# Kernel optimization log

Measured on AMD Instinct MI355X. Metric: run time of the kernel, lower is better.

## Reference

```python
import jax, jax.numpy as jnp
import numpy as np

N_SUM, N_MAX, M, HID, OUT, E, L = 2048, 64, 16, 128, 64, 16384, 4


def setup_inputs() -> dict:
    key = jax.random.key(0)
    ks = jax.random.split(key, 8)
    inp = {}
    inp["W"] = jax.random.normal(ks[0], (N_SUM, N_MAX, M), jnp.float32)
    inp["mask"] = jnp.ones((N_SUM, N_MAX), jnp.float32)
    inp["src"] = jax.random.randint(ks[1], (E,), 0, N_SUM)
    inp["dst"] = jax.random.randint(ks[2], (E,), 0, N_SUM)
    # GIN parameters: per-layer eps, MLP (Linear -> BN -> ReLU -> Linear)
    inp["eps"] = jax.random.normal(ks[3], (L,), jnp.float32)
    inp["W1_first"] = jax.random.normal(ks[4], (M, HID), jnp.float32) / np.sqrt(M).astype(np.float32)
    inp["b1_first"] = jnp.zeros((HID,), jnp.float32)
    inp["W1_rest"] = jax.random.normal(ks[5], (L - 1, HID, HID), jnp.float32) / np.sqrt(HID).astype(np.float32)
    inp["b1_rest"] = jnp.zeros((L - 1, HID), jnp.float32)
    inp["bn_gamma"] = jnp.ones((L, HID), jnp.float32)
    inp["bn_beta"] = jnp.zeros((L, HID), jnp.float32)
    inp["W2_mid"] = jax.random.normal(ks[6], (L - 1, HID, HID), jnp.float32) / np.sqrt(HID).astype(np.float32)
    inp["b2_mid"] = jnp.zeros((L - 1, HID), jnp.float32)
    inp["W2_last"] = jax.random.normal(ks[7], (HID, OUT), jnp.float32) / np.sqrt(HID).astype(np.float32)
    inp["b2_last"] = jnp.zeros((OUT,), jnp.float32)
    return inp


def _batchnorm(Hf, gamma, beta):
    # training-mode BatchNorm1d over flattened leading dims (biased variance)
    mu = Hf.mean(axis=0)
    var = Hf.var(axis=0)
    return (Hf - mu) * jax.lax.rsqrt(var + 1e-5) * gamma + beta


def _gin_layer(X, src, dst, eps, W1, b1, gamma, beta, W2, b2):
    # scatter-add message passing: gather sources, segment-sum into targets
    S = jax.ops.segment_sum(X[src], dst, num_segments=X.shape[0])  # [N_sum, n_max, D]
    Z = (1.0 + eps) * X + S
    H = Z @ W1 + b1                     # [N_sum, n_max, HID]
    shp = H.shape
    H = _batchnorm(H.reshape(-1, shp[-1]), gamma, beta)
    H = jax.nn.relu(H).reshape(shp)
    return H @ W2 + b2


def reference(W, mask, src, dst, eps, W1_first, b1_first, W1_rest, b1_rest,
              bn_gamma, bn_beta, W2_mid, b2_mid, W2_last, b2_last):
    X = W
    for l in range(L):
        W1 = W1_first if l == 0 else W1_rest[l - 1]
        b1 = b1_first if l == 0 else b1_rest[l - 1]
        W2 = W2_mid[l] if l < L - 1 else W2_last
        b2 = b2_mid[l] if l < L - 1 else b2_last
        X = _gin_layer(X, src, dst, eps[l], W1, b1, bn_gamma[l], bn_beta[l], W2, b2)
    # masked sum over the padded node axis -> positional encodings [N_sum, OUT]
    PE = (X * mask[:, :, None]).sum(axis=1)
    return PE
```

## Files before the change

kernel.cpp:

```cpp
#include <hip/hip_runtime.h>

#define N_SUM 2048
#define HIDD 128
#define NEDGE 16384
#define ROWS (N_SUM * 64)
#define NSLOT 16

typedef short short8 __attribute__((ext_vector_type(8)));
typedef float floatx4 __attribute__((ext_vector_type(4)));
typedef unsigned int uint4n __attribute__((ext_vector_type(4)));
typedef unsigned short ushort_t;

__device__ __forceinline__ ushort_t f2bf(float f) {
    unsigned u = __builtin_bit_cast(unsigned, f);
    u += 0x7fffu + ((u >> 16) & 1u);
    return (ushort_t)(u >> 16);
}
__device__ __forceinline__ float bf2f(ushort_t h) {
    return __builtin_bit_cast(float, (unsigned)h << 16);
}
__device__ __forceinline__ void unpack8(uint4 v, float* f) {
    f[0] = bf2f(v.x & 0xffff); f[1] = bf2f(v.x >> 16);
    f[2] = bf2f(v.y & 0xffff); f[3] = bf2f(v.y >> 16);
    f[4] = bf2f(v.z & 0xffff); f[5] = bf2f(v.z >> 16);
    f[6] = bf2f(v.w & 0xffff); f[7] = bf2f(v.w >> 16);
}
__device__ __forceinline__ uint4 pack8(const float* f) {
    uint4 v;
    v.x = f2bf(f[0]) | ((unsigned)f2bf(f[1]) << 16);
    v.y = f2bf(f[2]) | ((unsigned)f2bf(f[3]) << 16);
    v.z = f2bf(f[4]) | ((unsigned)f2bf(f[5]) << 16);
    v.w = f2bf(f[6]) | ((unsigned)f2bf(f[7]) << 16);
    return v;
}
__device__ __forceinline__ void nt_store16(const void* src, void* dst) {
    __builtin_nontemporal_store(*(const uint4n*)src, (uint4n*)dst);
}

__global__ __launch_bounds__(1024) void mega_prep(const int* __restrict__ src, const int* __restrict__ dst,
                                                  const float* __restrict__ W1f, const float* __restrict__ W2l,
                                                  const float* __restrict__ b2m, const float* __restrict__ W1r,
                                                  const float* __restrict__ W2m,
                                                  int* __restrict__ irp, int* __restrict__ icol,
                                                  ushort_t* __restrict__ w1t0, ushort_t* __restrict__ w2lt,
                                                  float* __restrict__ bvec, ushort_t* __restrict__ w21t,
                                                  float* __restrict__ sums) {
    __shared__ int sdeg[2048];
    __shared__ int scur[2048];
    __shared__ int red[1024];
    int tid = threadIdx.x, blk = blockIdx.x;

    if (blk == 0) {
        sdeg[tid] = 0;
        sdeg[tid + 1024] = 0;
        __syncthreads();
        int d[16];
#pragma unroll
        for (int q = 0; q < 16; q++) d[q] = dst[q * 1024 + tid];
#pragma unroll
        for (int q = 0; q < 16; q++) atomicAdd(&sdeg[d[q]], 1);
        __syncthreads();
        int a = sdeg[2 * tid], b = sdeg[2 * tid + 1];
        red[tid] = a + b;
        __syncthreads();
        for (int off = 1; off < 1024; off <<= 1) {
            int v = (tid >= off) ? red[tid - off] : 0;
            __syncthreads();
            red[tid] += v;
            __syncthreads();
        }
        int base = (tid == 0) ? 0 : red[tid - 1];
        irp[2 * tid] = base;
        irp[2 * tid + 1] = base + a;
        scur[2 * tid] = base;
        scur[2 * tid + 1] = base + a;
        if (tid == 1023) irp[2048] = red[1023];
        __syncthreads();
        int s[16];
#pragma unroll
        for (int q = 0; q < 16; q++) s[q] = src[q * 1024 + tid];
#pragma unroll
        for (int q = 0; q < 16; q++) {
            int pos = atomicAdd(&scur[d[q]], 1);
            icol[pos] = s[q];
        }
    } else if (blk <= 13) {
        int idx = (blk - 1) * 1024 + tid;
        if (idx < 4096) {
            int nn = idx >> 5, k = idx & 31;
            w1t0[idx] = f2bf(k < 16 ? W1f[k * 128 + nn] : 0.f);
        } else if (idx < 4096 + 8192) {
            int r = idx - 4096;
            int nn = r >> 7, k = r & 127;
            w2lt[r] = f2bf(W2l[k * 64 + nn]);
        } else if (idx < 4096 + 8192 + 384) {
            int r = idx - 12288;
            int lm = r >> 7, c = r & 127;
            float s = 0.f;
            for (int o = 0; o < 128; o++) s += b2m[lm * 128 + o] * W1r[(size_t)lm * 16384 + o * 128 + c];
            bvec[r] = s;
        }
    } else if (blk <= 61) {
        int idx = (blk - 14) * 1024 + tid;
        int lm = idx >> 14, r = idx & 16383, i = r >> 7, c = r & 127;
        const float* w2row = W2m + (size_t)lm * 16384 + i * 128;
        const float* w1col = W1r + (size_t)lm * 16384 + c;
        float s = 0.f;
#pragma unroll 8
        for (int o = 0; o < 128; o++) s += w2row[o] * w1col[o * 128];
        w21t[(size_t)lm * 16384 + c * 128 + i] = f2bf(s);
    } else {
        int idx = (blk - 62) * 1024 + tid;
#pragma unroll
        for (int q = 0; q < 8; q++) sums[idx * 8 + q] = 0.f;
    }
}


__global__ __launch_bounds__(256, 4) void gin_mm1_l0(const float* __restrict__ Xf, const ushort_t* __restrict__ W1t,
                                                     const float* __restrict__ b1, const float* __restrict__ eps,
                                                     const int* __restrict__ rp, const int* __restrict__ colv,
                                                     ushort_t* __restrict__ H, float* __restrict__ sums) {
    __shared__ ushort_t Zs[64 * 128];
    int tid = threadIdx.x, n = blockIdx.x;
    float ev = 1.0f + eps[0];
    int e0 = rp[n], e1 = rp[n + 1], deg = e1 - e0;
    const float4* X = (const float4*)Xf;

    float4 sA, sB;
    sA = X[(size_t)n * 256 + tid];
    if (deg > 0) sB = X[(size_t)colv[e0] * 256 + tid];
    float4 a;
    a.x = sA.x * ev; a.y = sA.y * ev; a.z = sA.z * ev; a.w = sA.w * ev;
    int i = 1;
    for (; i + 1 < deg; i += 2) {
        sA = X[(size_t)colv[e0 + i] * 256 + tid];
        a.x += sB.x; a.y += sB.y; a.z += sB.z; a.w += sB.w;
        sB = X[(size_t)colv[e0 + i + 1] * 256 + tid];
        a.x += sA.x; a.y += sA.y; a.z += sA.z; a.w += sA.w;
    }
    if (deg > 0) {
        if (i < deg) {
            sA = X[(size_t)colv[e0 + i] * 256 + tid];
            a.x += sB.x; a.y += sB.y; a.z += sB.z; a.w += sB.w;
            a.x += sA.x; a.y += sA.y; a.z += sA.z; a.w += sA.w;
        } else {
            a.x += sB.x; a.y += sB.y; a.z += sB.z; a.w += sB.w;
        }
    }

    {
        int m = tid >> 2, k0 = (tid & 3) * 4;
        int addr = ((k0 >> 3) * 64 + m) * 8 + (k0 & 7);
        uint2 pv;
        pv.x = f2bf(a.x) | ((unsigned)f2bf(a.y) << 16);
        pv.y = f2bf(a.z) | ((unsigned)f2bf(a.w) << 16);
        *(uint2*)&Zs[addr] = pv;
        *(uint2*)&Zs[1024 + tid * 4] = make_uint2(0u, 0u);
    }
    __syncthreads();

    int w = tid >> 6, lane = tid & 63, lg = lane >> 4, ln = lane & 15;
    floatx4 C[4][2];
#pragma unroll
    for (int mt = 0; mt < 4; mt++) { C[mt][0] = {0.f, 0.f, 0.f, 0.f}; C[mt][1] = {0.f, 0.f, 0.f, 0.f}; }

    {
        short8 B0 = *(const short8*)&W1t[(w * 32 + ln) * 32 + lg * 8];
        short8 B1 = *(const short8*)&W1t[(w * 32 + 16 + ln) * 32 + lg * 8];
#pragma unroll
        for (int mt = 0; mt < 4; mt++) {
            short8 A = *(const short8*)&Zs[(lg * 64 + mt * 16 + ln) * 8];
            C[mt][0] = __builtin_amdgcn_mfma_f32_16x16x32_bf16(A, B0, C[mt][0], 0, 0, 0);
            C[mt][1] = __builtin_amdgcn_mfma_f32_16x16x32_bf16(A, B1, C[mt][1], 0, 0, 0);
        }
    }

    float bsum[2], bsq[2];
    float bv[2] = {b1[w * 32 + ln], b1[w * 32 + 16 + ln]};
#pragma unroll
    for (int nt = 0; nt < 2; nt++) {
        float s = 0.f, s2 = 0.f;
#pragma unroll
        for (int mt = 0; mt < 4; mt++)
#pragma unroll
            for (int r = 0; r < 4; r++) {
                float v = C[mt][nt][r] + bv[nt];
                C[mt][nt][r] = v;
                s += v; s2 += v * v;
            }
        bsum[nt] = s; bsq[nt] = s2;
    }
#pragma unroll
    for (int nt = 0; nt < 2; nt++) {
        bsum[nt] += __shfl_xor(bsum[nt], 16, 64);
        bsum[nt] += __shfl_xor(bsum[nt], 32, 64);
        bsq[nt] += __shfl_xor(bsq[nt], 16, 64);
        bsq[nt] += __shfl_xor(bsq[nt], 32, 64);
    }
    if (lg == 0) {
        float* sl = sums + (n & (NSLOT - 1)) * 256;
        int c0 = w * 32 + ln;
        atomicAdd(&sl[c0], bsum[0]);
        atomicAdd(&sl[c0 + 16], bsum[1]);
        atomicAdd(&sl[128 + c0], bsq[0]);
        atomicAdd(&sl[128 + c0 + 16], bsq[1]);
    }
    __syncthreads();
#pragma unroll
    for (int nt = 0; nt < 2; nt++) {
        int colc = w * 32 + nt * 16 + ln;
        int base = (colc >> 3) * 512 + (colc & 7);
#pragma unroll
        for (int mt = 0; mt < 4; mt++)
#pragma unroll
            for (int r = 0; r < 4; r++) {
                int row = mt * 16 + lg * 4 + r;
                Zs[base + row * 8] = f2bf(C[mt][nt][r]);
            }
    }
    __syncthreads();
#pragma unroll
    for (int q = 0; q < 4; q++)
        nt_store16(&((const uint4*)Zs)[q * 256 + tid], &((uint4*)&H[(size_t)n * 8192])[q * 256 + tid]);
}

__global__ __launch_bounds__(512, 4) void gin_mm1_fused(const ushort_t* __restrict__ Hin,
                                                        const ushort_t* __restrict__ W21t,
                                                        const float* __restrict__ b1, const float* __restrict__ bvec,
                                                        const float* __restrict__ sums_prev,
                                                        const float* __restrict__ gam_prev,
                                                        const float* __restrict__ bet_prev,
                                                        const float* __restrict__ epsp,
                                                        const int* __restrict__ rp, const int* __restrict__ colv,
                                                        ushort_t* __restrict__ Hout, float* __restrict__ sums_cur) {
    __shared__ ushort_t Zs[64 * 128];
    __shared__ float scs_lds[256];
    int tid = threadIdx.x, n = blockIdx.x;
    if (tid < 128) {
        float s = 0.f, s2 = 0.f;
#pragma unroll
        for (int k = 0; k < NSLOT; k++) {
            s += sums_prev[k * 256 + tid];
            s2 += sums_prev[k * 256 + 128 + tid];
        }
        float mean = s * (1.f / (float)ROWS);
        float var = s2 * (1.f / (float)ROWS) - mean * mean;
        float sc = gam_prev[tid] * rsqrtf(var + 1e-5f);
        scs_lds[tid] = sc;
        scs_lds[128 + tid] = bet_prev[tid] - mean * sc;
    }
    __syncthreads();

    unsigned scp[2][8];
#pragma unroll
    for (int q = 0; q < 2; q++) {
        int cb = ((q * 512 + tid) >> 6) * 8;
#pragma unroll
        for (int j = 0; j < 8; j++)
            scp[q][j] = ((unsigned)f2bf(scs_lds[cb + j])) | ((unsigned)f2bf(scs_lds[128 + cb + j]) << 16);
    }

    float ev = 1.0f + epsp[0];
    int e0 = rp[n], e1 = rp[n + 1], deg = e1 - e0;
    const uint4* X = (const uint4*)Hin;
    float acc[2][8];
    uint4 bufA[2], bufB[2];

    auto loadslab = [&](uint4* buf, int node) {
        const uint4* p = X + (size_t)node * 1024;
        buf[0] = p[tid];
        buf[1] = p[512 + tid];
    };
    auto addp = [&](const uint4* buf) {
#pragma unroll
        for (int q = 0; q < 2; q++) {
            float f[8]; unpack8(buf[q], f);
#pragma unroll
            for (int j = 0; j < 8; j++) {
                float sc = __builtin_bit_cast(float, scp[q][j] << 16);
                float sh = __builtin_bit_cast(float, scp[q][j] & 0xffff0000u);
                acc[q][j] += fmaxf(fmaf(f[j], sc, sh), 0.f);
            }
        }
    };

    loadslab(bufA, n);
    if (deg > 0) loadslab(bufB, colv[e0]);

#pragma unroll
    for (int q = 0; q < 2; q++) {
        float f[8]; unpack8(bufA[q], f);
#pragma unroll
        for (int j = 0; j < 8; j++) {
            float sc = __builtin_bit_cast(float, scp[q][j] << 16);
            float sh = __builtin_bit_cast(float, scp[q][j] & 0xffff0000u);
            acc[q][j] = ev * fmaxf(fmaf(f[j], sc, sh), 0.f);
        }
    }

    int i = 1;
    for (; i + 1 < deg; i += 2) {
        loadslab(bufA, colv[e0 + i]);
        addp(bufB);
        loadslab(bufB, colv[e0 + i + 1]);
        addp(bufA);
    }
    if (deg > 0) {
        if (i < deg) {
            loadslab(bufA, colv[e0 + i]);
            addp(bufB);
            addp(bufA);
        } else {
            addp(bufB);
        }
    }

#pragma unroll
    for (int q = 0; q < 2; q++) ((uint4*)Zs)[q * 512 + tid] = pack8(acc[q]);
    __syncthreads();

    int w = tid >> 6, lane = tid & 63, lg = lane >> 4, ln = lane & 15;
    floatx4 C[4];
#pragma unroll
    for (int mt = 0; mt < 4; mt++) C[mt] = {0.f, 0.f, 0.f, 0.f};

    for (int kb = 0; kb < 4; kb++) {
        short8 B = *(const short8*)&W21t[(w * 16 + ln) * 128 + kb * 32 + lg * 8];
#pragma unroll
        for (int mt = 0; mt < 4; mt++) {
            short8 A = *(const short8*)&Zs[((kb * 4 + lg) * 64 + mt * 16 + ln) * 8];
            C[mt] = __builtin_amdgcn_mfma_f32_16x16x32_bf16(A, B, C[mt], 0, 0, 0);
        }
    }

    float fac = ev + (float)deg;
    int c0 = w * 16 + ln;
    float bv = b1[c0] + fac * bvec[c0];
    float s = 0.f, s2 = 0.f;
#pragma unroll
    for (int mt = 0; mt < 4; mt++)
#pragma unroll
        for (int r = 0; r < 4; r++) {
            float v = C[mt][r] + bv;
            C[mt][r] = v;
            s += v; s2 += v * v;
        }
    s += __shfl_xor(s, 16, 64);
    s += __shfl_xor(s, 32, 64);
    s2 += __shfl_xor(s2, 16, 64);
    s2 += __shfl_xor(s2, 32, 64);
    if (lg == 0) {
        float* sl = sums_cur + (n & (NSLOT - 1)) * 256;
        atomicAdd(&sl[c0], s);
        atomicAdd(&sl[128 + c0], s2);
    }

    __syncthreads();
    {
        int base = (c0 >> 3) * 512 + (c0 & 7);
#pragma unroll
        for (int mt = 0; mt < 4; mt++)
#pragma unroll
            for (int r = 0; r < 4; r++) {
                int row = mt * 16 + lg * 4 + r;
                Zs[base + row * 8] = f2bf(C[mt][r]);
            }
    }
    __syncthreads();
#pragma unroll
    for (int q = 0; q < 2; q++)
        nt_store16(&((const uint4*)Zs)[q * 512 + tid], &((uint4*)&Hout[(size_t)n * 8192])[q * 512 + tid]);
}

__global__ __launch_bounds__(256, 4) void gin_mm2_last(const ushort_t* __restrict__ H, const ushort_t* __restrict__ W2t,
                                                       const float* __restrict__ b2,
                                                       const float* __restrict__ sums_prev,
                                                       const float* __restrict__ gam_prev,
                                                       const float* __restrict__ bet_prev,
                                                       const float* __restrict__ mask, float* __restrict__ out) {
    __shared__ ushort_t Hs[64 * 128];
    __shared__ float scs_lds[256];
    int tid = threadIdx.x, n = blockIdx.x;
    if (tid < 128) {
        float s = 0.f, s2 = 0.f;
#pragma unroll
        for (int k = 0; k < NSLOT; k++) {
            s += sums_prev[k * 256 + tid];
            s2 += sums_prev[k * 256 + 128 + tid];
        }
        float mean = s * (1.f / (float)ROWS);
        float var = s2 * (1.f / (float)ROWS) - mean * mean;
        float sc = gam_prev[tid] * rsqrtf(var + 1e-5f);
        scs_lds[tid] = sc;
        scs_lds[128 + tid] = bet_prev[tid] - mean * sc;
    }
    __syncthreads();

#pragma unroll
    for (int q = 0; q < 4; q++) {
        int c = q * 256 + tid;
        uint4 v = ((const uint4*)&H[(size_t)n * 8192])[c];
        float f[8]; unpack8(v, f);
        int cb = (c >> 6) * 8;
#pragma unroll
        for (int j = 0; j < 8; j++) f[j] = fmaxf(fmaf(f[j], scs_lds[cb + j], scs_lds[128 + cb + j]), 0.f);
        ((uint4*)Hs)[c] = pack8(f);
    }
    __syncthreads();

    int w = tid >> 6, lane = tid & 63, lg = lane >> 4, ln = lane & 15;
    floatx4 C[4];
#pragma unroll
    for (int mt = 0; mt < 4; mt++) C[mt] = {0.f, 0.f, 0.f, 0.f};

    for (int kb = 0; kb < 4; kb++) {
        short8 B = *(const short8*)&W2t[(w * 16 + ln) * 128 + kb * 32 + lg * 8];
#pragma unroll
        for (int mt = 0; mt < 4; mt++) {
            short8 A = *(const short8*)&Hs[((kb * 4 + lg) * 64 + mt * 16 + ln) * 8];
            C[mt] = __builtin_amdgcn_mfma_f32_16x16x32_bf16(A, B, C[mt], 0, 0, 0);
        }
    }

    int colc = w * 16 + ln;
    float bb = b2[colc];
    float pe = 0.f;
#pragma unroll
    for (int mt = 0; mt < 4; mt++)
#pragma unroll
        for (int r = 0; r < 4; r++) {
            int row = mt * 16 + lg * 4 + r;
            pe += mask[n * 64 + row] * (C[mt][r] + bb);
        }
    pe += __shfl_xor(pe, 16, 64);
    pe += __shfl_xor(pe, 32, 64);
    if (lg == 0) out[(size_t)n * 64 + colc] = pe;
}

extern "C" void kernel_launch(void* const* d_in, const int* in_sizes, int n_in, void* d_out, int out_size,
                              void* d_ws, size_t ws_size, hipStream_t stream) {
    const float* W    = (const float*)d_in[0];
    const float* mask = (const float*)d_in[1];
    const int* src    = (const int*)d_in[2];
    const int* dst    = (const int*)d_in[3];
    const float* eps  = (const float*)d_in[4];
    const float* W1f  = (const float*)d_in[5];
    const float* b1f  = (const float*)d_in[6];
    const float* W1r  = (const float*)d_in[7];
    const float* b1r  = (const float*)d_in[8];
    const float* gam  = (const float*)d_in[9];
    const float* bet  = (const float*)d_in[10];
    const float* W2m  = (const float*)d_in[11];
    const float* b2m  = (const float*)d_in[12];
    const float* W2l  = (const float*)d_in[13];
    const float* b2l  = (const float*)d_in[14];
    float* out = (float*)d_out;

    ushort_t* Ha   = (ushort_t*)d_ws;
    ushort_t* Hb   = Ha + 16777216;
    ushort_t* w1t0 = Hb + 16777216;
    ushort_t* w2lt = w1t0 + 4096;
    ushort_t* w21t = w2lt + 8192;
    float* bvec    = (float*)(w21t + 49152);
    float* sums    = bvec + 384;
    int* irp       = (int*)(sums + 16384);
    int* icol      = irp + 2052;

    mega_prep<<<64, 1024, 0, stream>>>(src, dst, W1f, W2l, b2m, W1r, W2m, irp, icol,
                                       w1t0, w2lt, bvec, w21t, sums);

    const int SL = NSLOT * 256;
    gin_mm1_l0<<<N_SUM, 256, 0, stream>>>(W, w1t0, b1f, eps, irp, icol, Ha, sums);
    gin_mm1_fused<<<N_SUM, 512, 0, stream>>>(Ha, w21t, b1r, bvec, sums, gam, bet, eps + 1,
                                             irp, icol, Hb, sums + SL);
    gin_mm1_fused<<<N_SUM, 512, 0, stream>>>(Hb, w21t + 16384, b1r + 128, bvec + 128, sums + SL,
                                             gam + 128, bet + 128, eps + 2, irp, icol, Ha, sums + 2 * SL);
    gin_mm1_fused<<<N_SUM, 512, 0, stream>>>(Ha, w21t + 32768, b1r + 256, bvec + 256, sums + 2 * SL,
                                             gam + 256, bet + 256, eps + 3, irp, icol, Hb, sums + 3 * SL);
    gin_mm2_last<<<N_SUM, 256, 0, stream>>>(Hb, w2lt, b2l, sums + 3 * SL, gam + 384, bet + 384, mask, out);
}
```

Before: 263.7 us.

## Pad CSR neighbor lists to multiples of four and gather four slabs in flight

Each node's adjacency list is padded to a multiple of four with a sentinel node index that points to an all-zero slab appended to each H buffer. The fused layer kernels now keep four neighbor slab loads in flight instead of two, so more memory latency is overlapped during the gather. Padded entries go through the BN/ReLU transform like real neighbors, and their contribution (relu of the shift term) is subtracted afterwards using the true degree. The cost is extra gather traffic for the padding, larger register use, and a small amount of extra setup work in the prep kernel.

```diff
diff --git a/kernel.cpp b/kernel.cpp
--- a/kernel.cpp
+++ b/kernel.cpp
@@ -5,6 +5,8 @@
 #define NEDGE 16384
 #define ROWS (N_SUM * 64)
 #define NSLOT 16
+#define SLAB 8192
+#define SENT 2048
 
 typedef short short8 __attribute__((ext_vector_type(8)));
 typedef float floatx4 __attribute__((ext_vector_type(4)));
@@ -42,9 +44,11 @@
                                                   const float* __restrict__ b2m, const float* __restrict__ W1r,
                                                   const float* __restrict__ W2m,
                                                   int* __restrict__ irp, int* __restrict__ icol,
+                                                  int* __restrict__ idegv,
                                                   ushort_t* __restrict__ w1t0, ushort_t* __restrict__ w2lt,
                                                   float* __restrict__ bvec, ushort_t* __restrict__ w21t,
-                                                  float* __restrict__ sums) {
+                                                  float* __restrict__ sums,
+                                                  ushort_t* __restrict__ Ha, ushort_t* __restrict__ Hb) {
     __shared__ int sdeg[2048];
     __shared__ int scur[2048];
     __shared__ int red[1024];
@@ -61,7 +65,8 @@
         for (int q = 0; q < 16; q++) atomicAdd(&sdeg[d[q]], 1);
         __syncthreads();
         int a = sdeg[2 * tid], b = sdeg[2 * tid + 1];
-        red[tid] = a + b;
+        int ap = (a + 3) & ~3, bp = (b + 3) & ~3;
+        red[tid] = ap + bp;
         __syncthreads();
         for (int off = 1; off < 1024; off <<= 1) {
             int v = (tid >= off) ? red[tid - off] : 0;
@@ -71,9 +76,13 @@
         }
         int base = (tid == 0) ? 0 : red[tid - 1];
         irp[2 * tid] = base;
-        irp[2 * tid + 1] = base + a;
+        irp[2 * tid + 1] = base + ap;
         scur[2 * tid] = base;
-        scur[2 * tid + 1] = base + a;
+        scur[2 * tid + 1] = base + ap;
+        idegv[2 * tid] = a;
+        idegv[2 * tid + 1] = b;
+        sdeg[2 * tid] = base + ap;
+        sdeg[2 * tid + 1] = base + ap + bp;
         if (tid == 1023) irp[2048] = red[1023];
         __syncthreads();
         int s[16];
@@ -83,6 +92,12 @@
         for (int q = 0; q < 16; q++) {
             int pos = atomicAdd(&scur[d[q]], 1);
             icol[pos] = s[q];
+        }
+        __syncthreads();
+#pragma unroll
+        for (int q = 0; q < 2; q++) {
+            int node = 2 * tid + q;
+            for (int p = scur[node]; p < sdeg[node]; p++) icol[p] = SENT;
         }
     } else if (blk <= 13) {
         int idx = (blk - 1) * 1024 + tid;
@@ -109,22 +124,26 @@
 #pragma unroll 8
         for (int o = 0; o < 128; o++) s += w2row[o] * w1col[o * 128];
         w21t[(size_t)lm * 16384 + c * 128 + i] = f2bf(s);
+    } else if (blk == 62) {
+#pragma unroll
+        for (int q = 0; q < 16; q++) sums[tid * 16 + q] = 0.f;
     } else {
-        int idx = (blk - 62) * 1024 + tid;
-#pragma unroll
-        for (int q = 0; q < 8; q++) sums[idx * 8 + q] = 0.f;
+        uint4 z = make_uint4(0u, 0u, 0u, 0u);
+        ((uint4*)(Ha + (size_t)SENT * SLAB))[tid] = z;
+        ((uint4*)(Hb + (size_t)SENT * SLAB))[tid] = z;
     }
 }
 
 
 __global__ __launch_bounds__(256, 4) void gin_mm1_l0(const float* __restrict__ Xf, const ushort_t* __restrict__ W1t,
                                                      const float* __restrict__ b1, const float* __restrict__ eps,
-                                                     const int* __restrict__ rp, const int* __restrict__ colv,
+                                                     const int* __restrict__ rp, const int* __restrict__ idegv,
+                                                     const int* __restrict__ colv,
                                                      ushort_t* __restrict__ H, float* __restrict__ sums) {
     __shared__ ushort_t Zs[64 * 128];
     int tid = threadIdx.x, n = blockIdx.x;
     float ev = 1.0f + eps[0];
-    int e0 = rp[n], e1 = rp[n + 1], deg = e1 - e0;
+    int e0 = rp[n], deg = idegv[n];
     const float4* X = (const float4*)Xf;
 
     float4 sA, sB;
@@ -222,7 +241,7 @@
     __syncthreads();
 #pragma unroll
     for (int q = 0; q < 4; q++)
-        nt_store16(&((const uint4*)Zs)[q * 256 + tid], &((uint4*)&H[(size_t)n * 8192])[q * 256 + tid]);
+        nt_store16(&((const uint4*)Zs)[q * 256 + tid], &((uint4*)&H[(size_t)n * SLAB])[q * 256 + tid]);
 }
 
 __global__ __launch_bounds__(512, 4) void gin_mm1_fused(const ushort_t* __restrict__ Hin,
@@ -232,7 +251,8 @@
                                                         const float* __restrict__ gam_prev,
                                                         const float* __restrict__ bet_prev,
                                                         const float* __restrict__ epsp,
-                                                        const int* __restrict__ rp, const int* __restrict__ colv,
+                                                        const int* __restrict__ rp, const int* __restrict__ idegv,
+                                                        const int* __restrict__ colv,
                                                         ushort_t* __restrict__ Hout, float* __restrict__ sums_cur) {
     __shared__ ushort_t Zs[64 * 128];
     __shared__ float scs_lds[256];
@@ -262,10 +282,10 @@
     }
 
     float ev = 1.0f + epsp[0];
-    int e0 = rp[n], e1 = rp[n + 1], deg = e1 - e0;
+    int e0 = rp[n], degp = rp[n + 1] - e0, deg = idegv[n];
     const uint4* X = (const uint4*)Hin;
     float acc[2][8];
-    uint4 bufA[2], bufB[2];
+    uint4 bufS[2], r0[2], r1[2], r2[2], r3[2];
 
     auto loadslab = [&](uint4* buf, int node) {
         const uint4* p = X + (size_t)node * 1024;
@@ -285,12 +305,17 @@
         }
     };
 
-    loadslab(bufA, n);
-    if (deg > 0) loadslab(bufB, colv[e0]);
+    loadslab(bufS, n);
+    if (degp > 0) {
+        loadslab(r0, colv[e0]);
+        loadslab(r1, colv[e0 + 1]);
+        loadslab(r2, colv[e0 + 2]);
+        loadslab(r3, colv[e0 + 3]);
+    }
 
 #pragma unroll
     for (int q = 0; q < 2; q++) {
-        float f[8]; unpack8(bufA[q], f);
+        float f[8]; unpack8(bufS[q], f);
 #pragma unroll
         for (int j = 0; j < 8; j++) {
             float sc = __builtin_bit_cast(float, scp[q][j] << 16);
@@ -299,20 +324,24 @@
         }
     }
 
-    int i = 1;
-    for (; i + 1 < deg; i += 2) {
-        loadslab(bufA, colv[e0 + i]);
-        addp(bufB);
-        loadslab(bufB, colv[e0 + i + 1]);
-        addp(bufA);
-    }
-    if (deg > 0) {
-        if (i < deg) {
-            loadslab(bufA, colv[e0 + i]);
-            addp(bufB);
-            addp(bufA);
-        } else {
-            addp(bufB);
+    if (degp > 0) {
+        for (int e = 4; e < degp; e += 4) {
+            addp(r0); loadslab(r0, colv[e0 + e]);
+            addp(r1); loadslab(r1, colv[e0 + e + 1]);
+            addp(r2); loadslab(r2, colv[e0 + e + 2]);
+            addp(r3); loadslab(r3, colv[e0 + e + 3]);
+        }
+        addp(r0); addp(r1); addp(r2); addp(r3);
+        int npad = degp - deg;
+        if (npad > 0) {
+            float fnp = (float)npad;
+#pragma unroll
+            for (int q = 0; q < 2; q++)
+#pragma unroll
+                for (int j = 0; j < 8; j++) {
+                    float sh = __builtin_bit_cast(float, scp[q][j] & 0xffff0000u);
+                    acc[q][j] -= fnp * fmaxf(sh, 0.f);
+                }
         }
     }
 
@@ -370,7 +399,7 @@
     __syncthreads();
 #pragma unroll
     for (int q = 0; q < 2; q++)
-        nt_store16(&((const uint4*)Zs)[q * 512 + tid], &((uint4*)&Hout[(size_t)n * 8192])[q * 512 + tid]);
+        nt_store16(&((const uint4*)Zs)[q * 512 + tid], &((uint4*)&Hout[(size_t)n * SLAB])[q * 512 + tid]);
 }
 
 __global__ __launch_bounds__(256, 4) void gin_mm2_last(const ushort_t* __restrict__ H, const ushort_t* __restrict__ W2t,
@@ -400,7 +429,7 @@
 #pragma unroll
     for (int q = 0; q < 4; q++) {
         int c = q * 256 + tid;
-        uint4 v = ((const uint4*)&H[(size_t)n * 8192])[c];
+        uint4 v = ((const uint4*)&H[(size_t)n * SLAB])[c];
         float f[8]; unpack8(v, f);
         int cb = (c >> 6) * 8;
 #pragma unroll
@@ -457,26 +486,28 @@
     const float* b2l  = (const float*)d_in[14];
     float* out = (float*)d_out;
 
+    const size_t HSZ = (size_t)2049 * SLAB;
     ushort_t* Ha   = (ushort_t*)d_ws;
-    ushort_t* Hb   = Ha + 16777216;
-    ushort_t* w1t0 = Hb + 16777216;
+    ushort_t* Hb   = Ha + HSZ;
+    ushort_t* w1t0 = Hb + HSZ;
     ushort_t* w2lt = w1t0 + 4096;
     ushort_t* w21t = w2lt + 8192;
     float* bvec    = (float*)(w21t + 49152);
     float* sums    = bvec + 384;
-    int* irp       = (int*)(sums + 16384);
+    int* idegv     = (int*)(sums + 16384);
+    int* irp       = idegv + 2048;
     int* icol      = irp + 2052;
 
-    mega_prep<<<64, 1024, 0, stream>>>(src, dst, W1f, W2l, b2m, W1r, W2m, irp, icol,
-                                       w1t0, w2lt, bvec, w21t, sums);
+    mega_prep<<<64, 1024, 0, stream>>>(src, dst, W1f, W2l, b2m, W1r, W2m, irp, icol, idegv,
+                                       w1t0, w2lt, bvec, w21t, sums, Ha, Hb);
 
     const int SL = NSLOT * 256;
-    gin_mm1_l0<<<N_SUM, 256, 0, stream>>>(W, w1t0, b1f, eps, irp, icol, Ha, sums);
+    gin_mm1_l0<<<N_SUM, 256, 0, stream>>>(W, w1t0, b1f, eps, irp, idegv, icol, Ha, sums);
     gin_mm1_fused<<<N_SUM, 512, 0, stream>>>(Ha, w21t, b1r, bvec, sums, gam, bet, eps + 1,
-                                             irp, icol, Hb, sums + SL);
+                                             irp, idegv, icol, Hb, sums + SL);
     gin_mm1_fused<<<N_SUM, 512, 0, stream>>>(Hb, w21t + 16384, b1r + 128, bvec + 128, sums + SL,
-                                             gam + 128, bet + 128, eps + 2, irp, icol, Ha, sums + 2 * SL);
+                                             gam + 128, bet + 128, eps + 2, irp, idegv, icol, Ha, sums + 2 * SL);
     gin_mm1_fused<<<N_SUM, 512, 0, stream>>>(Ha, w21t + 32768, b1r + 256, bvec + 256, sums + 2 * SL,
-                                             gam + 256, bet + 256, eps + 3, irp, icol, Hb, sums + 3 * SL);
+                                             gam + 256, bet + 256, eps + 3, irp, idegv, icol, Hb, sums + 3 * SL);
     gin_mm2_last<<<N_SUM, 256, 0, stream>>>(Hb, w2lt, b2l, sums + 3 * SL, gam + 384, bet + 384, mask, out);
 }
```

After: 265.8 us. No clear change (+0.8%).
